# Optimization experiments

Hardware: AMD Instinct MI355X
Metric: run time of the kernel (lower is better)

The kernel has to match this reference:

```python
import jax, jax.numpy as jnp
import numpy as np

N, E, H, IN = 4096, 65536, 256, 16
N_BLOCKS, N_SUB = 3, 2
IE = 2 * H + 2  # edge-mlp input: h[row] ++ h[col] ++ edge_attr(2)
NORM_FACTOR = 100.0


def setup_inputs() -> dict:
    key = jax.random.key(0)
    ks = jax.random.split(key, 24)
    G = N_BLOCKS * N_SUB  # 6 GCLs total

    def p(k, shape, fan_in, gain=1.0):
        return gain * jax.random.normal(k, shape, jnp.float32) / np.sqrt(fan_in)

    return {
        "h": jax.random.normal(ks[0], (N, IN), jnp.float32),
        "x": jax.random.normal(ks[1], (N, 3), jnp.float32),
        "edge_index": jax.random.randint(ks[2], (2, E), 0, N),
        # embedding in/out
        "emb_w": p(ks[3], (IN, H), IN), "emb_b": jnp.zeros((H,), jnp.float32),
        "out_w": p(ks[4], (H, IN), H), "out_b": jnp.zeros((IN,), jnp.float32),
        # GCL edge MLP (stacked over the 6 GCLs)
        "edge_w1": p(ks[5], (G, IE, H), IE), "edge_b1": jnp.zeros((G, H), jnp.float32),
        "edge_w2": p(ks[6], (G, H, H), H), "edge_b2": jnp.zeros((G, H), jnp.float32),
        # GCL node MLP
        "node_w1": p(ks[7], (G, 2 * H, H), 2 * H), "node_b1": jnp.zeros((G, H), jnp.float32),
        "node_w2": p(ks[8], (G, H, H), H), "node_b2": jnp.zeros((G, H), jnp.float32),
        # EquivariantUpdate coord MLP (stacked over 3 blocks); last layer xavier gain=0.001, no bias
        "coord_w1": p(ks[9], (N_BLOCKS, IE, H), IE), "coord_b1": jnp.zeros((N_BLOCKS, H), jnp.float32),
        "coord_w2": p(ks[10], (N_BLOCKS, H, H), H), "coord_b2": jnp.zeros((N_BLOCKS, H), jnp.float32),
        "coord_w3": p(ks[11], (N_BLOCKS, H, 1), H, gain=0.001),
    }


def reference(h, x, edge_index, emb_w, emb_b, out_w, out_b,
              edge_w1, edge_b1, edge_w2, edge_b2,
              node_w1, node_b1, node_w2, node_b2,
              coord_w1, coord_b1, coord_w2, coord_b2, coord_w3):
    row, col = edge_index[0], edge_index[1]
    n_nodes = h.shape[0]

    def seg_sum(data):  # unsorted_segment_sum with 'sum' aggregation / normalization_factor
        return jax.ops.segment_sum(data, row, num_segments=n_nodes) / NORM_FACTOR

    def coord2diff(xc):  # norm_constant = 1
        d = xc[row] - xc[col]                      # [E,3]
        radial = jnp.sum(d * d, axis=1, keepdims=True)  # [E,1]
        cd = d / (jnp.sqrt(radial + 1e-8) + 1.0)
        return radial, cd

    dist0, _ = coord2diff(x)          # EGNN-level distances (from initial coords)
    h = h @ emb_w + emb_b             # node embedding

    gi = 0
    for b in range(N_BLOCKS):
        radial, coord_diff = coord2diff(x)
        ea = jnp.concatenate([radial, dist0], axis=1)   # [E,2] edge_attr
        for _ in range(N_SUB):  # GCL sublayers
            m = jnp.concatenate([h[row], h[col], ea], axis=1)           # [E, 2H+2]
            m = jax.nn.silu(m @ edge_w1[gi] + edge_b1[gi])
            m = jax.nn.silu(m @ edge_w2[gi] + edge_b2[gi])              # [E, H]
            agg = seg_sum(m)                                            # [N, H]
            u = jnp.concatenate([h, agg], axis=1)                       # [N, 2H]
            u = jax.nn.silu(u @ node_w1[gi] + node_b1[gi])
            h = h + u @ node_w2[gi] + node_b2[gi]                       # residual node update
            gi += 1
        # EquivariantUpdate (tanh=False)
        t = jnp.concatenate([h[row], h[col], ea], axis=1)
        t = jax.nn.silu(t @ coord_w1[b] + coord_b1[b])
        t = jax.nn.silu(t @ coord_w2[b] + coord_b2[b])
        trans = coord_diff * (t @ coord_w3[b])                          # [E,3]
        x = x + seg_sum(trans)

    h = h @ out_w + out_b
    return h, x
```

## Files before the change

### kernel.cpp

```cpp
#include <hip/hip_runtime.h>
#include <hip/hip_bf16.h>
#include <cstdint>
#include <cstddef>

#define NN 4096
#define NE 65536
#define HD 256

typedef __attribute__((ext_vector_type(4))) float f32x4;
typedef __attribute__((ext_vector_type(8))) __bf16 bf16x8;

static __device__ __forceinline__ float silu_f(float v) {
  float e = __builtin_amdgcn_exp2f(v * -1.442695040888963f);
  return v * __builtin_amdgcn_rcpf(1.f + e);
}

struct TJob { const float* src; __bf16* dst; int K; int N; };
struct TJobs { TJob j[39]; };

__global__ __launch_bounds__(256) void k_transpose(TJobs jobs) {
  TJob jb = jobs.j[blockIdx.z];
  int k0 = blockIdx.x << 5, n0 = blockIdx.y << 5;
  if (k0 >= jb.K || n0 >= jb.N) return;
  __shared__ float t[32][33];
  int tx = threadIdx.x & 31, ty = threadIdx.x >> 5;
#pragma unroll
  for (int r = ty; r < 32; r += 8)
    t[r][tx] = jb.src[(size_t)(k0 + r) * jb.N + n0 + tx];
  __syncthreads();
#pragma unroll
  for (int r = ty; r < 32; r += 8)
    jb.dst[(size_t)(n0 + r) * jb.K + k0 + tx] = (__bf16)t[tx][r];
}

__global__ __launch_bounds__(256) void k_hist(const int* __restrict__ ei, int* __restrict__ cnt) {
  int e = blockIdx.x * 256 + threadIdx.x;
  atomicAdd(&cnt[ei[e]], 1);
}

__global__ __launch_bounds__(1024) void k_scan(const int* __restrict__ cnt, int* __restrict__ offs,
                                               int* __restrict__ cursor) {
  __shared__ int tmp[1024];
  int tid = threadIdx.x;
  int v[4]; int s = 0;
#pragma unroll
  for (int i = 0; i < 4; i++) { v[i] = cnt[tid * 4 + i]; s += v[i]; }
  tmp[tid] = s;
  __syncthreads();
  for (int o = 1; o < 1024; o <<= 1) {
    int t = (tid >= o) ? tmp[tid - o] : 0;
    __syncthreads();
    tmp[tid] += t;
    __syncthreads();
  }
  int base = (tid > 0) ? tmp[tid - 1] : 0;
#pragma unroll
  for (int i = 0; i < 4; i++) {
    offs[tid * 4 + i] = base; cursor[tid * 4 + i] = base; base += v[i];
  }
  if (tid == 1023) offs[4096] = base;
}

__global__ __launch_bounds__(256) void k_scatter(const int* __restrict__ ei, int* __restrict__ cursor,
                                                 int* __restrict__ elist) {
  int e = blockIdx.x * 256 + threadIdx.x;
  int pos = atomicAdd(&cursor[ei[e]], 1);
  elist[pos] = e;
}

__global__ __launch_bounds__(256) void k_csrinit(const int* __restrict__ elist, const int* __restrict__ ei,
                                                 const float* __restrict__ x, int* __restrict__ rowp,
                                                 int* __restrict__ colp, float* __restrict__ d0p,
                                                 float* __restrict__ xc) {
  int i = blockIdx.x * 256 + threadIdx.x;
  if (i < NN * 3) xc[i] = x[i];
  int e = elist[i];
  int r = ei[e], c = ei[NE + e];
  rowp[i] = r; colp[i] = c;
  float dx = x[r * 3 + 0] - x[c * 3 + 0];
  float dy = x[r * 3 + 1] - x[c * 3 + 1];
  float dz = x[r * 3 + 2] - x[c * 3 + 2];
  d0p[i] = dx * dx + dy * dy + dz * dz;
}

__global__ __launch_bounds__(256) void k_geo(const int* __restrict__ rowp, const int* __restrict__ colp,
                                             const float* __restrict__ x, float* __restrict__ radp,
                                             float* __restrict__ cdp) {
  int i = blockIdx.x * 256 + threadIdx.x;
  int r = rowp[i], c = colp[i];
  float dx = x[r * 3 + 0] - x[c * 3 + 0];
  float dy = x[r * 3 + 1] - x[c * 3 + 1];
  float dz = x[r * 3 + 2] - x[c * 3 + 2];
  float rad = dx * dx + dy * dy + dz * dz;
  radp[i] = rad;
  float inv = 1.f / (sqrtf(rad + 1e-8f) + 1.f);
  cdp[i * 3 + 0] = dx * inv; cdp[i * 3 + 1] = dy * inv; cdp[i * 3 + 2] = dz * inv;
}

__global__ __launch_bounds__(256) void k_embed(const float* __restrict__ h0, const float* __restrict__ W,
                                               const float* __restrict__ b, float* __restrict__ hf,
                                               __bf16* __restrict__ h16) {
  int n = blockIdx.x, c = threadIdx.x;
  float s = b[c];
#pragma unroll
  for (int i = 0; i < 16; i++) s += h0[n * 16 + i] * W[i * 256 + c];
  hf[(size_t)n * HD + c] = s;
  h16[(size_t)n * HD + c] = (__bf16)s;
}

__global__ __launch_bounds__(256) void k_mkbias(const float* __restrict__ eb1, const float* __restrict__ cb1,
                                                float* __restrict__ bias512) {
  int i = blockIdx.x * 256 + threadIdx.x;
  int g = i >> 9, r = i & 511;
  float v = 0.f;
  if (r < 256) v = (g < 6) ? eb1[g * 256 + r] : cb1[(g - 6) * 256 + r];
  bias512[i] = v;
}

__global__ __launch_bounds__(256) void k_segsum(const __bf16* __restrict__ m2p, const int* __restrict__ offs,
                                                __bf16* __restrict__ agg16) {
  __shared__ float sd[8][256];
  int n = blockIdx.x, t = threadIdx.x;
  int g = t >> 5, l = t & 31;
  int c0 = l << 3;
  float a[8] = {};
  int ib = offs[n], ie = offs[n + 1];
  for (int i = ib + g; i < ie; i += 8) {
    bf16x8 v = *(const bf16x8*)(m2p + (size_t)i * 256 + c0);
#pragma unroll
    for (int j = 0; j < 8; j++) a[j] += (float)v[j];
  }
#pragma unroll
  for (int j = 0; j < 8; j++) sd[g][c0 + j] = a[j];
  __syncthreads();
  float s = 0.f;
#pragma unroll
  for (int j = 0; j < 8; j++) s += sd[j][t];
  agg16[(size_t)n * 256 + t] = (__bf16)(s * 0.01f);
}

__global__ __launch_bounds__(256) void k_xupd(const float* __restrict__ transp, const int* __restrict__ offs,
                                              float* __restrict__ xc) {
  int n = blockIdx.x * 256 + threadIdx.x;
  if (n >= NN) return;
  float a0 = 0.f, a1 = 0.f, a2 = 0.f;
  int i1 = offs[n + 1];
  for (int i = offs[n]; i < i1; i++) {
    a0 += transp[i * 3 + 0]; a1 += transp[i * 3 + 1]; a2 += transp[i * 3 + 2];
  }
  xc[n * 3 + 0] += a0 * 0.01f;
  xc[n * 3 + 1] += a1 * 0.01f;
  xc[n * 3 + 2] += a2 * 0.01f;
}

__global__ __launch_bounds__(256) void k_out(const float* __restrict__ hf, const float* __restrict__ W,
                                             const float* __restrict__ b, const float* __restrict__ xc,
                                             float* __restrict__ out) {
  int t = blockIdx.x * 256 + threadIdx.x;
  if (blockIdx.x < 256) {
    int n = t >> 4, j = t & 15;
    float s = b[j];
    for (int c = 0; c < 256; c++) s += hf[(size_t)n * HD + c] * W[c * 16 + j];
    out[n * 16 + j] = s;
  } else {
    int i = t - NN * 16;
    if (i < NN * 3) out[NN * 16 + i] = xc[i];
  }
}

template <int EPI>
__global__ __launch_bounds__(512, 4) void k_edgeblk(
    const __bf16* __restrict__ PQ, const int* __restrict__ rowp, const int* __restrict__ colp,
    const float* __restrict__ radp, const float* __restrict__ d0p,
    const float* __restrict__ w1r, const float* __restrict__ w1d,
    const __bf16* __restrict__ Bt, const float* __restrict__ b2,
    __bf16* __restrict__ m2p,
    const float* __restrict__ w3, const float* __restrict__ cdp, float* __restrict__ transp) {
  __shared__ alignas(16) char smem[37888];
  float*  wgt = (float*)smem;
  __bf16* Bs0 = (__bf16*)(smem + 4096);
  __bf16* Bs1 = (__bf16*)(smem + 4096 + 16384);
  float*  reds = (float*)(smem + 4096);

  const int tid = threadIdx.x;
  const int lane = tid & 63;
  const int w = tid >> 6;
  const int l15 = lane & 15;
  const int kg = lane >> 4;
  const int R0 = blockIdx.x * 128;
  const int rowg = R0 + w * 16 + l15;

  const __bf16* pBase = PQ + (size_t)rowp[rowg] * 512;
  const __bf16* qBase = PQ + (size_t)colp[rowg] * 512 + 256;
  const float rad = radp[rowg], dd0 = d0p[rowg];

  if (tid < 256) {
    wgt[tid]       = w1r[tid];
    wgt[256 + tid] = w1d[tid];
  } else {
    int t2 = tid - 256;
    wgt[512 + t2] = b2[t2];
    if (EPI == 1) wgt[768 + t2] = w3[t2];
  }

  int srcOff[2];
#pragma unroll
  for (int q = 0; q < 2; q++) {
    int s = q * 512 + tid;
    int n = s >> 2, g = s & 3;
    srcOff[q] = n * 256 + ((g ^ ((n >> 1) & 3)) << 3);
  }
  const int dstE0 = (0 * 512 + (w << 6)) * 8;
  const int dstE1 = (1 * 512 + (w << 6)) * 8;

  __builtin_amdgcn_global_load_lds((const unsigned int*)(Bt + srcOff[0]),
                                   (unsigned int*)(Bs0 + dstE0), 16, 0, 0);
  __builtin_amdgcn_global_load_lds((const unsigned int*)(Bt + srcOff[1]),
                                   (unsigned int*)(Bs0 + dstE1), 16, 0, 0);
  bf16x8 pvc = *(const bf16x8*)(pBase + kg * 8);
  bf16x8 qvc = *(const bf16x8*)(qBase + kg * 8);
  __syncthreads();

  f32x4 acc[16] = {};

#pragma unroll
  for (int t = 0; t < 8; t++) {
    const __bf16* Bcur = (t & 1) ? Bs1 : Bs0;
    __bf16*       Bnxt = (t & 1) ? Bs0 : Bs1;
    bf16x8 pvn, qvn;
    if (t < 7) {
      int kt = (t + 1) * 32;
      __builtin_amdgcn_global_load_lds((const unsigned int*)(Bt + kt + srcOff[0]),
                                       (unsigned int*)(Bnxt + dstE0), 16, 0, 0);
      __builtin_amdgcn_global_load_lds((const unsigned int*)(Bt + kt + srcOff[1]),
                                       (unsigned int*)(Bnxt + dstE1), 16, 0, 0);
      pvn = *(const bf16x8*)(pBase + kt + kg * 8);
      qvn = *(const bf16x8*)(qBase + kt + kg * 8);
    }
    const int k0 = t * 32 + kg * 8;
    f32x4 wr0 = *(const f32x4*)&wgt[k0],       wr1 = *(const f32x4*)&wgt[k0 + 4];
    f32x4 wd0 = *(const f32x4*)&wgt[256 + k0], wd1 = *(const f32x4*)&wgt[256 + k0 + 4];
    bf16x8 af;
#pragma unroll
    for (int j = 0; j < 4; j++)
      af[j] = (__bf16)silu_f((float)pvc[j] + (float)qvc[j] + rad * wr0[j] + dd0 * wd0[j]);
#pragma unroll
    for (int j = 0; j < 4; j++)
      af[4 + j] = (__bf16)silu_f((float)pvc[4 + j] + (float)qvc[4 + j] + rad * wr1[j] + dd0 * wd1[j]);
    __builtin_amdgcn_s_setprio(1);
#pragma unroll
    for (int fn = 0; fn < 16; fn++) {
      int n = fn * 16 + l15;
      bf16x8 bf = *(const bf16x8*)&Bcur[n * 32 + ((kg ^ ((n >> 1) & 3)) << 3)];
      acc[fn] = __builtin_amdgcn_mfma_f32_16x16x32_bf16(af, bf, acc[fn], 0, 0, 0);
    }
    __builtin_amdgcn_s_setprio(0);
    if (t < 7) { pvc = pvn; qvc = qvn; }
    __syncthreads();
  }

  if (EPI == 0) {
    __bf16* ep = (__bf16*)(smem + 4096 + w * 4224);
#pragma unroll
    for (int p = 0; p < 2; p++) {
      if ((kg >> 1) == p) {
        int rl = (kg & 1) * 4;
#pragma unroll
        for (int fn = 0; fn < 16; fn++) {
          int col = fn * 16 + l15;
          float bv = wgt[512 + col];
#pragma unroll
          for (int j = 0; j < 4; j++)
            ep[(rl + j) * 264 + col] = (__bf16)silu_f(acc[fn][j] + bv);
        }
      }
      __syncthreads();
#pragma unroll
      for (int i = 0; i < 4; i++) {
        int r = i * 2 + (lane >> 5);
        int g = lane & 31;
        uint4 v = *(const uint4*)&ep[r * 264 + g * 8];
        *(uint4*)(m2p + ((size_t)(R0 + w * 16 + p * 8 + r)) * 256 + g * 8) = v;
      }
      __syncthreads();
    }
  } else {
    float s[4] = {0.f, 0.f, 0.f, 0.f};
#pragma unroll
    for (int fn = 0; fn < 16; fn++) {
      int col = fn * 16 + l15;
      float bv = wgt[512 + col], wv = wgt[768 + col];
#pragma unroll
      for (int j = 0; j < 4; j++)
        s[j] += silu_f(acc[fn][j] + bv) * wv;
    }
#pragma unroll
    for (int off = 1; off < 16; off <<= 1)
#pragma unroll
      for (int j = 0; j < 4; j++)
        s[j] += __shfl_xor(s[j], off, 64);
    __syncthreads();
    if (l15 == 0) {
#pragma unroll
      for (int j = 0; j < 4; j++)
        reds[w * 16 + kg * 4 + j] = s[j];
    }
    __syncthreads();
    if (tid < 128) {
      float sv = reds[tid];
      size_t i = (size_t)R0 + tid;
      transp[i * 3 + 0] = cdp[i * 3 + 0] * sv;
      transp[i * 3 + 1] = cdp[i * 3 + 1] * sv;
      transp[i * 3 + 2] = cdp[i * 3 + 2] * sv;
    }
  }
}

template <int EPI, int SPLIT>
__global__ __launch_bounds__(256) void k_gemm64(const __bf16* __restrict__ A, const __bf16* __restrict__ A2,
                                                const __bf16* __restrict__ Bt,
                                                const float* __restrict__ bias, __bf16* __restrict__ outb,
                                                float* __restrict__ outf, int M, int N, int K) {
  constexpr int BM = 64, BN = 64, BK = 64;
  __shared__ __bf16 As[2][BM * BK];
  __shared__ __bf16 Bs[2][BN * BK];
  const int tid = threadIdx.x;
  const int lane = tid & 63;
  const int wave = tid >> 6;
  const int wm = wave >> 1, wn = wave & 1;
  const size_t m0 = (size_t)blockIdx.x * BM;
  const size_t n0 = (size_t)blockIdx.y * BN;
  const int r0 = tid >> 3, g0 = tid & 7;
  const int gs0 = (g0 ^ (r0 & 7)) << 3;
  const int Astride = SPLIT ? 256 : K;

  f32x4 acc[2][2] = {};
  const int NT = K >> 6;

  {
    uint4 a0 = *(const uint4*)(A + (m0 + r0) * Astride + g0 * 8);
    uint4 a1 = *(const uint4*)(A + (m0 + r0 + 32) * Astride + g0 * 8);
    uint4 b0 = *(const uint4*)(Bt + (n0 + r0) * K + g0 * 8);
    uint4 b1 = *(const uint4*)(Bt + (n0 + r0 + 32) * K + g0 * 8);
    *(uint4*)&As[0][r0 * BK + gs0] = a0;
    *(uint4*)&As[0][(r0 + 32) * BK + gs0] = a1;
    *(uint4*)&Bs[0][r0 * BK + gs0] = b0;
    *(uint4*)&Bs[0][(r0 + 32) * BK + gs0] = b1;
  }
  __syncthreads();

  int buf = 0;
  for (int t = 0; t < NT; ++t) {
    const bool has = (t + 1 < NT);
    uint4 a0, a1, b0, b1;
    if (has) {
      int kt = (t + 1) << 6;
      const __bf16* Ab;
      int ko;
      if (SPLIT) { Ab = (kt < 256) ? A : A2; ko = kt & 255; }
      else       { Ab = A; ko = kt; }
      a0 = *(const uint4*)(Ab + (m0 + r0) * Astride + ko + g0 * 8);
      a1 = *(const uint4*)(Ab + (m0 + r0 + 32) * Astride + ko + g0 * 8);
      b0 = *(const uint4*)(Bt + (n0 + r0) * K + kt + g0 * 8);
      b1 = *(const uint4*)(Bt + (n0 + r0 + 32) * K + kt + g0 * 8);
    }
#pragma unroll
    for (int ks = 0; ks < BK; ks += 32) {
      const int kg = (ks >> 3) + (lane >> 4);
      bf16x8 af[2], bfv[2];
#pragma unroll
      for (int fm = 0; fm < 2; fm++) {
        int r = wm * 32 + fm * 16 + (lane & 15);
        af[fm] = *(const bf16x8*)&As[buf][r * BK + ((kg ^ (r & 7)) << 3)];
      }
#pragma unroll
      for (int fn = 0; fn < 2; fn++) {
        int r = wn * 32 + fn * 16 + (lane & 15);
        bfv[fn] = *(const bf16x8*)&Bs[buf][r * BK + ((kg ^ (r & 7)) << 3)];
      }
#pragma unroll
      for (int fm = 0; fm < 2; fm++)
#pragma unroll
        for (int fn = 0; fn < 2; fn++)
          acc[fm][fn] = __builtin_amdgcn_mfma_f32_16x16x32_bf16(af[fm], bfv[fn], acc[fm][fn], 0, 0, 0);
    }
    if (has) {
      *(uint4*)&As[buf ^ 1][r0 * BK + gs0] = a0;
      *(uint4*)&As[buf ^ 1][(r0 + 32) * BK + gs0] = a1;
      *(uint4*)&Bs[buf ^ 1][r0 * BK + gs0] = b0;
      *(uint4*)&Bs[buf ^ 1][(r0 + 32) * BK + gs0] = b1;
    }
    __syncthreads();
    buf ^= 1;
  }

#pragma unroll
  for (int fm = 0; fm < 2; fm++) {
#pragma unroll
    for (int fn = 0; fn < 2; fn++) {
      const size_t col = n0 + wn * 32 + fn * 16 + (lane & 15);
      float bv = (EPI == 4) ? 0.f : bias[col];
#pragma unroll
      for (int j = 0; j < 4; j++) {
        size_t row = m0 + wm * 32 + fm * 16 + ((lane >> 4) << 2) + j;
        size_t idx = row * (size_t)N + col;
        float v = acc[fm][fn][j] + bv;
        if (EPI == 1) {
          outb[idx] = (__bf16)silu_f(v);
        } else if (EPI == 2) {
          float nh = outf[idx] + v;
          outf[idx] = nh;
          outb[idx] = (__bf16)nh;
        } else {
          outb[idx] = (__bf16)v;
        }
      }
    }
  }
}

extern "C" void kernel_launch(void* const* d_in, const int* in_sizes, int n_in,
                              void* d_out, int out_size, void* d_ws, size_t ws_size,
                              hipStream_t stream) {
  const float* h_in    = (const float*)d_in[0];
  const float* x_in    = (const float*)d_in[1];
  const int*   ei      = (const int*)d_in[2];
  const float* emb_w   = (const float*)d_in[3];
  const float* emb_b   = (const float*)d_in[4];
  const float* out_w   = (const float*)d_in[5];
  const float* out_b   = (const float*)d_in[6];
  const float* edge_w1 = (const float*)d_in[7];
  const float* edge_b1 = (const float*)d_in[8];
  const float* edge_w2 = (const float*)d_in[9];
  const float* edge_b2 = (const float*)d_in[10];
  const float* node_w1 = (const float*)d_in[11];
  const float* node_b1 = (const float*)d_in[12];
  const float* node_w2 = (const float*)d_in[13];
  const float* node_b2 = (const float*)d_in[14];
  const float* coord_w1 = (const float*)d_in[15];
  const float* coord_b1 = (const float*)d_in[16];
  const float* coord_w2 = (const float*)d_in[17];
  const float* coord_b2 = (const float*)d_in[18];
  const float* coord_w3 = (const float*)d_in[19];

  char* p = (char*)d_ws;
  auto alloc = [&](size_t bytes) -> void* {
    void* r = (void*)p;
    p += (bytes + 255) & ~(size_t)255;
    return r;
  };
  __bf16* e1T  = (__bf16*)alloc((size_t)6 * 512 * 256 * 2);
  __bf16* e2T  = (__bf16*)alloc((size_t)6 * 256 * 256 * 2);
  __bf16* n1T  = (__bf16*)alloc((size_t)6 * 256 * 512 * 2);
  __bf16* n2T  = (__bf16*)alloc((size_t)6 * 256 * 256 * 2);
  __bf16* c1T  = (__bf16*)alloc((size_t)3 * 512 * 256 * 2);
  __bf16* c2T  = (__bf16*)alloc((size_t)3 * 256 * 256 * 2);
  __bf16* h16  = (__bf16*)alloc((size_t)NN * HD * 2);
  __bf16* PQ16 = (__bf16*)alloc((size_t)NN * 512 * 2);
  __bf16* m2p  = (__bf16*)alloc((size_t)NE * HD * 2);
  __bf16* agg16 = (__bf16*)alloc((size_t)NN * HD * 2);
  __bf16* u    = (__bf16*)alloc((size_t)NN * HD * 2);
  float* hf    = (float*)alloc((size_t)NN * HD * 4);
  float* xc    = (float*)alloc((size_t)NN * 3 * 4);
  float* d0p   = (float*)alloc((size_t)NE * 4);
  float* radp  = (float*)alloc((size_t)NE * 4);
  float* cdp   = (float*)alloc((size_t)NE * 3 * 4);
  float* transp = (float*)alloc((size_t)NE * 3 * 4);
  float* bias512 = (float*)alloc((size_t)9 * 512 * 4);
  int* cnt     = (int*)alloc((size_t)NN * 4);
  int* offs    = (int*)alloc((size_t)(NN + 1) * 4);
  int* cursor  = (int*)alloc((size_t)NN * 4);
  int* elist   = (int*)alloc((size_t)NE * 4);
  int* rowp    = (int*)alloc((size_t)NE * 4);
  int* colp    = (int*)alloc((size_t)NE * 4);

  TJobs jobs;
  int nj = 0;
  for (int gi = 0; gi < 6; gi++) {
    jobs.j[nj++] = { edge_w1 + (size_t)gi * 514 * 256,             e1T + (size_t)gi * 512 * 256,             256, 256 };
    jobs.j[nj++] = { edge_w1 + (size_t)gi * 514 * 256 + 256 * 256, e1T + (size_t)gi * 512 * 256 + 256 * 256, 256, 256 };
    jobs.j[nj++] = { edge_w2 + (size_t)gi * 256 * 256,             e2T + (size_t)gi * 256 * 256,             256, 256 };
    jobs.j[nj++] = { node_w1 + (size_t)gi * 512 * 256,             n1T + (size_t)gi * 256 * 512,             512, 256 };
    jobs.j[nj++] = { node_w2 + (size_t)gi * 256 * 256,             n2T + (size_t)gi * 256 * 256,             256, 256 };
  }
  for (int b = 0; b < 3; b++) {
    jobs.j[nj++] = { coord_w1 + (size_t)b * 514 * 256,             c1T + (size_t)b * 512 * 256,              256, 256 };
    jobs.j[nj++] = { coord_w1 + (size_t)b * 514 * 256 + 256 * 256, c1T + (size_t)b * 512 * 256 + 256 * 256,  256, 256 };
    jobs.j[nj++] = { coord_w2 + (size_t)b * 256 * 256,             c2T + (size_t)b * 256 * 256,              256, 256 };
  }

  hipMemsetAsync(cnt, 0, (size_t)NN * 4, stream);
  k_transpose<<<dim3(16, 8, 39), 256, 0, stream>>>(jobs);
  k_hist<<<NE / 256, 256, 0, stream>>>(ei, cnt);
  k_scan<<<1, 1024, 0, stream>>>(cnt, offs, cursor);
  k_scatter<<<NE / 256, 256, 0, stream>>>(ei, cursor, elist);
  k_csrinit<<<NE / 256, 256, 0, stream>>>(elist, ei, x_in, rowp, colp, d0p, xc);
  k_mkbias<<<18, 256, 0, stream>>>(edge_b1, coord_b1, bias512);
  k_embed<<<NN, 256, 0, stream>>>(h_in, emb_w, emb_b, hf, h16);

  int gi = 0;
  for (int b = 0; b < 3; b++) {
    k_geo<<<NE / 256, 256, 0, stream>>>(rowp, colp, xc, radp, cdp);
    for (int s = 0; s < 2; s++, gi++) {
      const float* w1 = edge_w1 + (size_t)gi * 514 * 256;
      k_gemm64<5, 0><<<dim3(64, 8), 256, 0, stream>>>(
          h16, nullptr, e1T + (size_t)gi * 512 * 256, bias512 + gi * 512, PQ16, nullptr, NN, 512, 256);
      k_edgeblk<0><<<NE / 128, 512, 0, stream>>>(
          PQ16, rowp, colp, radp, d0p, w1 + 512 * 256, w1 + 513 * 256,
          e2T + (size_t)gi * 256 * 256, edge_b2 + gi * 256, m2p, nullptr, nullptr, nullptr);
      k_segsum<<<NN, 256, 0, stream>>>(m2p, offs, agg16);
      k_gemm64<1, 1><<<dim3(64, 4), 256, 0, stream>>>(
          h16, agg16, n1T + (size_t)gi * 256 * 512, node_b1 + gi * 256, u, nullptr, NN, 256, 512);
      k_gemm64<2, 0><<<dim3(64, 4), 256, 0, stream>>>(
          u, nullptr, n2T + (size_t)gi * 256 * 256, node_b2 + gi * 256, h16, hf, NN, 256, 256);
    }
    const float* w1c = coord_w1 + (size_t)b * 514 * 256;
    k_gemm64<5, 0><<<dim3(64, 8), 256, 0, stream>>>(
        h16, nullptr, c1T + (size_t)b * 512 * 256, bias512 + (6 + b) * 512, PQ16, nullptr, NN, 512, 256);
    k_edgeblk<1><<<NE / 128, 512, 0, stream>>>(
        PQ16, rowp, colp, radp, d0p, w1c + 512 * 256, w1c + 513 * 256,
        c2T + (size_t)b * 256 * 256, coord_b2 + b * 256, nullptr,
        coord_w3 + (size_t)b * 256, cdp, transp);
    k_xupd<<<NN / 256, 256, 0, stream>>>(transp, offs, xc);
  }
  k_out<<<256 + 48, 256, 0, stream>>>(hf, out_w, out_b, xc, (float*)d_out);
}
```

Baseline: 460.0 us.

## Fuse segment-sum into edge MLP epilogue via fp32 atomics on sorted rows

```diff
diff --git a/kernel.cpp b/kernel.cpp
--- a/kernel.cpp
+++ b/kernel.cpp
@@ -9,6 +9,8 @@
 
 typedef __attribute__((ext_vector_type(4))) float f32x4;
 typedef __attribute__((ext_vector_type(8))) __bf16 bf16x8;
+typedef __attribute__((ext_vector_type(4))) __bf16 bf16x4;
+union U8 { bf16x8 h; uint4 u; };
 
 static __device__ __forceinline__ float silu_f(float v) {
   float e = __builtin_amdgcn_exp2f(v * -1.442695040888963f);
@@ -71,6 +73,7 @@
 __global__ __launch_bounds__(256) void k_csrinit(const int* __restrict__ elist, const int* __restrict__ ei,
                                                  const float* __restrict__ x, int* __restrict__ rowp,
                                                  int* __restrict__ colp, float* __restrict__ d0p,
+                                                 float* __restrict__ radp, float* __restrict__ cdp,
                                                  float* __restrict__ xc) {
   int i = blockIdx.x * 256 + threadIdx.x;
   if (i < NN * 3) xc[i] = x[i];
@@ -80,7 +83,11 @@
   float dx = x[r * 3 + 0] - x[c * 3 + 0];
   float dy = x[r * 3 + 1] - x[c * 3 + 1];
   float dz = x[r * 3 + 2] - x[c * 3 + 2];
-  d0p[i] = dx * dx + dy * dy + dz * dz;
+  float rad = dx * dx + dy * dy + dz * dz;
+  d0p[i] = rad;
+  radp[i] = rad;
+  float inv = 1.f / (sqrtf(rad + 1e-8f) + 1.f);
+  cdp[i * 3 + 0] = dx * inv; cdp[i * 3 + 1] = dy * inv; cdp[i * 3 + 2] = dz * inv;
 }
 
 __global__ __launch_bounds__(256) void k_geo(const int* __restrict__ rowp, const int* __restrict__ colp,
@@ -117,28 +124,6 @@
   bias512[i] = v;
 }
 
-__global__ __launch_bounds__(256) void k_segsum(const __bf16* __restrict__ m2p, const int* __restrict__ offs,
-                                                __bf16* __restrict__ agg16) {
-  __shared__ float sd[8][256];
-  int n = blockIdx.x, t = threadIdx.x;
-  int g = t >> 5, l = t & 31;
-  int c0 = l << 3;
-  float a[8] = {};
-  int ib = offs[n], ie = offs[n + 1];
-  for (int i = ib + g; i < ie; i += 8) {
-    bf16x8 v = *(const bf16x8*)(m2p + (size_t)i * 256 + c0);
-#pragma unroll
-    for (int j = 0; j < 8; j++) a[j] += (float)v[j];
-  }
-#pragma unroll
-  for (int j = 0; j < 8; j++) sd[g][c0 + j] = a[j];
-  __syncthreads();
-  float s = 0.f;
-#pragma unroll
-  for (int j = 0; j < 8; j++) s += sd[j][t];
-  agg16[(size_t)n * 256 + t] = (__bf16)(s * 0.01f);
-}
-
 __global__ __launch_bounds__(256) void k_xupd(const float* __restrict__ transp, const int* __restrict__ offs,
                                               float* __restrict__ xc) {
   int n = blockIdx.x * 256 + threadIdx.x;
@@ -174,7 +159,7 @@
     const float* __restrict__ radp, const float* __restrict__ d0p,
     const float* __restrict__ w1r, const float* __restrict__ w1d,
     const __bf16* __restrict__ Bt, const float* __restrict__ b2,
-    __bf16* __restrict__ m2p,
+    float* __restrict__ aggf,
     const float* __restrict__ w3, const float* __restrict__ cdp, float* __restrict__ transp) {
   __shared__ alignas(16) char smem[37888];
   float*  wgt = (float*)smem;
@@ -261,6 +246,7 @@
 
   if (EPI == 0) {
     __bf16* ep = (__bf16*)(smem + 4096 + w * 4224);
+    const int c0 = lane * 4;
 #pragma unroll
     for (int p = 0; p < 2; p++) {
       if ((kg >> 1) == p) {
@@ -275,12 +261,28 @@
         }
       }
       __syncthreads();
-#pragma unroll
-      for (int i = 0; i < 4; i++) {
-        int r = i * 2 + (lane >> 5);
-        int g = lane & 31;
-        uint4 v = *(const uint4*)&ep[r * 264 + g * 8];
-        *(uint4*)(m2p + ((size_t)(R0 + w * 16 + p * 8 + r)) * 256 + g * 8) = v;
+      {
+        const int base = R0 + w * 16 + p * 8;
+        int cur = rowp[base];
+        bf16x4 v0 = *(const bf16x4*)&ep[c0];
+        float s0 = (float)v0[0], s1 = (float)v0[1], s2 = (float)v0[2], s3 = (float)v0[3];
+#pragma unroll
+        for (int r = 1; r < 8; r++) {
+          int nid = rowp[base + r];
+          bf16x4 v = *(const bf16x4*)&ep[r * 264 + c0];
+          if (nid != cur) {
+            float* d = aggf + (size_t)cur * 256 + c0;
+            unsafeAtomicAdd(d + 0, s0); unsafeAtomicAdd(d + 1, s1);
+            unsafeAtomicAdd(d + 2, s2); unsafeAtomicAdd(d + 3, s3);
+            cur = nid;
+            s0 = (float)v[0]; s1 = (float)v[1]; s2 = (float)v[2]; s3 = (float)v[3];
+          } else {
+            s0 += (float)v[0]; s1 += (float)v[1]; s2 += (float)v[2]; s3 += (float)v[3];
+          }
+        }
+        float* d = aggf + (size_t)cur * 256 + c0;
+        unsafeAtomicAdd(d + 0, s0); unsafeAtomicAdd(d + 1, s1);
+        unsafeAtomicAdd(d + 2, s2); unsafeAtomicAdd(d + 3, s3);
       }
       __syncthreads();
     }
@@ -316,11 +318,12 @@
   }
 }
 
-template <int EPI, int SPLIT>
+template <int EPI, int SPLIT, int A2F>
 __global__ __launch_bounds__(256) void k_gemm64(const __bf16* __restrict__ A, const __bf16* __restrict__ A2,
                                                 const __bf16* __restrict__ Bt,
                                                 const float* __restrict__ bias, __bf16* __restrict__ outb,
-                                                float* __restrict__ outf, int M, int N, int K) {
+                                                float* __restrict__ outf, int M, int N, int K,
+                                                float* __restrict__ aggz) {
   constexpr int BM = 64, BN = 64, BK = 64;
   __shared__ __bf16 As[2][BM * BK];
   __shared__ __bf16 Bs[2][BN * BK];
@@ -334,6 +337,13 @@
   const int gs0 = (g0 ^ (r0 & 7)) << 3;
   const int Astride = SPLIT ? 256 : K;
 
+  if (EPI == 5 && aggz) {
+    int bid = blockIdx.y * gridDim.x + blockIdx.x;
+    float4 z = {0.f, 0.f, 0.f, 0.f};
+    float* dst = aggz + (size_t)bid * 2048 + tid * 8;
+    *(float4*)dst = z; *(float4*)(dst + 4) = z;
+  }
+
   f32x4 acc[2][2] = {};
   const int NT = K >> 6;
 
@@ -355,12 +365,25 @@
     uint4 a0, a1, b0, b1;
     if (has) {
       int kt = (t + 1) << 6;
-      const __bf16* Ab;
-      int ko;
-      if (SPLIT) { Ab = (kt < 256) ? A : A2; ko = kt & 255; }
-      else       { Ab = A; ko = kt; }
-      a0 = *(const uint4*)(Ab + (m0 + r0) * Astride + ko + g0 * 8);
-      a1 = *(const uint4*)(Ab + (m0 + r0 + 32) * Astride + ko + g0 * 8);
+      int ko = SPLIT ? (kt & 255) : kt;
+      if (SPLIT && A2F && kt >= 256) {
+        const float* af2 = (const float*)A2;
+        f32x4 u0 = *(const f32x4*)(af2 + (m0 + r0) * 256 + ko + g0 * 8);
+        f32x4 u1 = *(const f32x4*)(af2 + (m0 + r0) * 256 + ko + g0 * 8 + 4);
+        f32x4 u2 = *(const f32x4*)(af2 + (m0 + r0 + 32) * 256 + ko + g0 * 8);
+        f32x4 u3 = *(const f32x4*)(af2 + (m0 + r0 + 32) * 256 + ko + g0 * 8 + 4);
+        U8 x0, x1;
+#pragma unroll
+        for (int j = 0; j < 4; j++) {
+          x0.h[j] = (__bf16)(u0[j] * 0.01f); x0.h[4 + j] = (__bf16)(u1[j] * 0.01f);
+          x1.h[j] = (__bf16)(u2[j] * 0.01f); x1.h[4 + j] = (__bf16)(u3[j] * 0.01f);
+        }
+        a0 = x0.u; a1 = x1.u;
+      } else {
+        const __bf16* Ab = (SPLIT && kt >= 256) ? A2 : A;
+        a0 = *(const uint4*)(Ab + (m0 + r0) * Astride + ko + g0 * 8);
+        a1 = *(const uint4*)(Ab + (m0 + r0 + 32) * Astride + ko + g0 * 8);
+      }
       b0 = *(const uint4*)(Bt + (n0 + r0) * K + kt + g0 * 8);
       b1 = *(const uint4*)(Bt + (n0 + r0 + 32) * K + kt + g0 * 8);
     }
@@ -399,7 +422,7 @@
 #pragma unroll
     for (int fn = 0; fn < 2; fn++) {
       const size_t col = n0 + wn * 32 + fn * 16 + (lane & 15);
-      float bv = (EPI == 4) ? 0.f : bias[col];
+      float bv = bias[col];
 #pragma unroll
       for (int j = 0; j < 4; j++) {
         size_t row = m0 + wm * 32 + fm * 16 + ((lane >> 4) << 2) + j;
@@ -457,9 +480,8 @@
   __bf16* c2T  = (__bf16*)alloc((size_t)3 * 256 * 256 * 2);
   __bf16* h16  = (__bf16*)alloc((size_t)NN * HD * 2);
   __bf16* PQ16 = (__bf16*)alloc((size_t)NN * 512 * 2);
-  __bf16* m2p  = (__bf16*)alloc((size_t)NE * HD * 2);
-  __bf16* agg16 = (__bf16*)alloc((size_t)NN * HD * 2);
   __bf16* u    = (__bf16*)alloc((size_t)NN * HD * 2);
+  float* aggf  = (float*)alloc((size_t)NN * HD * 4);
   float* hf    = (float*)alloc((size_t)NN * HD * 4);
   float* xc    = (float*)alloc((size_t)NN * 3 * 4);
   float* d0p   = (float*)alloc((size_t)NE * 4);
@@ -494,34 +516,37 @@
   k_hist<<<NE / 256, 256, 0, stream>>>(ei, cnt);
   k_scan<<<1, 1024, 0, stream>>>(cnt, offs, cursor);
   k_scatter<<<NE / 256, 256, 0, stream>>>(ei, cursor, elist);
-  k_csrinit<<<NE / 256, 256, 0, stream>>>(elist, ei, x_in, rowp, colp, d0p, xc);
+  k_csrinit<<<NE / 256, 256, 0, stream>>>(elist, ei, x_in, rowp, colp, d0p, radp, cdp, xc);
   k_mkbias<<<18, 256, 0, stream>>>(edge_b1, coord_b1, bias512);
   k_embed<<<NN, 256, 0, stream>>>(h_in, emb_w, emb_b, hf, h16);
 
   int gi = 0;
   for (int b = 0; b < 3; b++) {
-    k_geo<<<NE / 256, 256, 0, stream>>>(rowp, colp, xc, radp, cdp);
     for (int s = 0; s < 2; s++, gi++) {
       const float* w1 = edge_w1 + (size_t)gi * 514 * 256;
-      k_gemm64<5, 0><<<dim3(64, 8), 256, 0, stream>>>(
-          h16, nullptr, e1T + (size_t)gi * 512 * 256, bias512 + gi * 512, PQ16, nullptr, NN, 512, 256);
+      k_gemm64<5, 0, 0><<<dim3(64, 8), 256, 0, stream>>>(
+          h16, nullptr, e1T + (size_t)gi * 512 * 256, bias512 + gi * 512, PQ16, nullptr,
+          NN, 512, 256, aggf);
       k_edgeblk<0><<<NE / 128, 512, 0, stream>>>(
           PQ16, rowp, colp, radp, d0p, w1 + 512 * 256, w1 + 513 * 256,
-          e2T + (size_t)gi * 256 * 256, edge_b2 + gi * 256, m2p, nullptr, nullptr, nullptr);
-      k_segsum<<<NN, 256, 0, stream>>>(m2p, offs, agg16);
-      k_gemm64<1, 1><<<dim3(64, 4), 256, 0, stream>>>(
-          h16, agg16, n1T + (size_t)gi * 256 * 512, node_b1 + gi * 256, u, nullptr, NN, 256, 512);
-      k_gemm64<2, 0><<<dim3(64, 4), 256, 0, stream>>>(
-          u, nullptr, n2T + (size_t)gi * 256 * 256, node_b2 + gi * 256, h16, hf, NN, 256, 256);
+          e2T + (size_t)gi * 256 * 256, edge_b2 + gi * 256, aggf, nullptr, nullptr, nullptr);
+      k_gemm64<1, 1, 1><<<dim3(64, 4), 256, 0, stream>>>(
+          h16, (const __bf16*)aggf, n1T + (size_t)gi * 256 * 512, node_b1 + gi * 256, u, nullptr,
+          NN, 256, 512, nullptr);
+      k_gemm64<2, 0, 0><<<dim3(64, 4), 256, 0, stream>>>(
+          u, nullptr, n2T + (size_t)gi * 256 * 256, node_b2 + gi * 256, h16, hf,
+          NN, 256, 256, nullptr);
     }
     const float* w1c = coord_w1 + (size_t)b * 514 * 256;
-    k_gemm64<5, 0><<<dim3(64, 8), 256, 0, stream>>>(
-        h16, nullptr, c1T + (size_t)b * 512 * 256, bias512 + (6 + b) * 512, PQ16, nullptr, NN, 512, 256);
+    k_gemm64<5, 0, 0><<<dim3(64, 8), 256, 0, stream>>>(
+        h16, nullptr, c1T + (size_t)b * 512 * 256, bias512 + (6 + b) * 512, PQ16, nullptr,
+        NN, 512, 256, nullptr);
     k_edgeblk<1><<<NE / 128, 512, 0, stream>>>(
         PQ16, rowp, colp, radp, d0p, w1c + 512 * 256, w1c + 513 * 256,
         c2T + (size_t)b * 256 * 256, coord_b2 + b * 256, nullptr,
         coord_w3 + (size_t)b * 256, cdp, transp);
     k_xupd<<<NN / 256, 256, 0, stream>>>(transp, offs, xc);
+    if (b < 2) k_geo<<<NE / 256, 256, 0, stream>>>(rowp, colp, xc, radp, cdp);
   }
   k_out<<<256 + 48, 256, 0, stream>>>(hf, out_w, out_b, xc, (float*)d_out);
 }
```

Result: slower. 608.0 us (+32.2%).

## Fuse node MLP GEMMs into single kernel with shared-memory intermediate

Applied to the files above, without the earlier changes.

```diff
diff --git a/kernel.cpp b/kernel.cpp
--- a/kernel.cpp
+++ b/kernel.cpp
@@ -316,11 +316,71 @@
   }
 }
 
-template <int EPI, int SPLIT>
-__global__ __launch_bounds__(256) void k_gemm64(const __bf16* __restrict__ A, const __bf16* __restrict__ A2,
+__global__ __launch_bounds__(512) void k_nodemlp(
+    const __bf16* __restrict__ h16, const __bf16* __restrict__ agg16,
+    const __bf16* __restrict__ W1t, const float* __restrict__ b1,
+    const __bf16* __restrict__ W2t, const float* __restrict__ b2,
+    __bf16* __restrict__ h16o, float* __restrict__ hf) {
+  __shared__ __bf16 us[16 * 264];
+  const int tid = threadIdx.x;
+  const int lane = tid & 63;
+  const int w = tid >> 6;
+  const int l15 = lane & 15;
+  const int kg = lane >> 4;
+  const int R0 = blockIdx.x * 16;
+  const int colb = w * 32;
+
+  f32x4 acc[2] = {};
+#pragma unroll
+  for (int ks = 0; ks < 16; ks++) {
+    const __bf16* Asrc = (ks < 8)
+        ? (h16  + (size_t)(R0 + l15) * 256 + ks * 32 + kg * 8)
+        : (agg16 + (size_t)(R0 + l15) * 256 + (ks - 8) * 32 + kg * 8);
+    bf16x8 av = *(const bf16x8*)Asrc;
+#pragma unroll
+    for (int fn = 0; fn < 2; fn++) {
+      bf16x8 bv = *(const bf16x8*)(W1t + (size_t)(colb + fn * 16 + l15) * 512 + ks * 32 + kg * 8);
+      acc[fn] = __builtin_amdgcn_mfma_f32_16x16x32_bf16(av, bv, acc[fn], 0, 0, 0);
+    }
+  }
+#pragma unroll
+  for (int fn = 0; fn < 2; fn++) {
+    int col = colb + fn * 16 + l15;
+    float bv = b1[col];
+#pragma unroll
+    for (int j = 0; j < 4; j++)
+      us[(kg * 4 + j) * 264 + col] = (__bf16)silu_f(acc[fn][j] + bv);
+  }
+  __syncthreads();
+
+  f32x4 acc2[2] = {};
+#pragma unroll
+  for (int ks = 0; ks < 8; ks++) {
+    bf16x8 av = *(const bf16x8*)&us[l15 * 264 + ks * 32 + kg * 8];
+#pragma unroll
+    for (int fn = 0; fn < 2; fn++) {
+      bf16x8 bv = *(const bf16x8*)(W2t + (size_t)(colb + fn * 16 + l15) * 256 + ks * 32 + kg * 8);
+      acc2[fn] = __builtin_amdgcn_mfma_f32_16x16x32_bf16(av, bv, acc2[fn], 0, 0, 0);
+    }
+  }
+#pragma unroll
+  for (int fn = 0; fn < 2; fn++) {
+    int col = colb + fn * 16 + l15;
+    float bv = b2[col];
+#pragma unroll
+    for (int j = 0; j < 4; j++) {
+      size_t idx = (size_t)(R0 + kg * 4 + j) * 256 + col;
+      float nh = hf[idx] + acc2[fn][j] + bv;
+      hf[idx] = nh;
+      h16o[idx] = (__bf16)nh;
+    }
+  }
+}
+
+__global__ __launch_bounds__(256) void k_gemm64(const __bf16* __restrict__ A,
                                                 const __bf16* __restrict__ Bt,
-                                                const float* __restrict__ bias, __bf16* __restrict__ outb,
-                                                float* __restrict__ outf, int M, int N, int K) {
+                                                const float* __restrict__ bias,
+                                                __bf16* __restrict__ outb, int M, int N, int K) {
   constexpr int BM = 64, BN = 64, BK = 64;
   __shared__ __bf16 As[2][BM * BK];
   __shared__ __bf16 Bs[2][BN * BK];
@@ -332,14 +392,13 @@
   const size_t n0 = (size_t)blockIdx.y * BN;
   const int r0 = tid >> 3, g0 = tid & 7;
   const int gs0 = (g0 ^ (r0 & 7)) << 3;
-  const int Astride = SPLIT ? 256 : K;
 
   f32x4 acc[2][2] = {};
   const int NT = K >> 6;
 
   {
-    uint4 a0 = *(const uint4*)(A + (m0 + r0) * Astride + g0 * 8);
-    uint4 a1 = *(const uint4*)(A + (m0 + r0 + 32) * Astride + g0 * 8);
+    uint4 a0 = *(const uint4*)(A + (m0 + r0) * K + g0 * 8);
+    uint4 a1 = *(const uint4*)(A + (m0 + r0 + 32) * K + g0 * 8);
     uint4 b0 = *(const uint4*)(Bt + (n0 + r0) * K + g0 * 8);
     uint4 b1 = *(const uint4*)(Bt + (n0 + r0 + 32) * K + g0 * 8);
     *(uint4*)&As[0][r0 * BK + gs0] = a0;
@@ -355,12 +414,8 @@
     uint4 a0, a1, b0, b1;
     if (has) {
       int kt = (t + 1) << 6;
-      const __bf16* Ab;
-      int ko;
-      if (SPLIT) { Ab = (kt < 256) ? A : A2; ko = kt & 255; }
-      else       { Ab = A; ko = kt; }
-      a0 = *(const uint4*)(Ab + (m0 + r0) * Astride + ko + g0 * 8);
-      a1 = *(const uint4*)(Ab + (m0 + r0 + 32) * Astride + ko + g0 * 8);
+      a0 = *(const uint4*)(A + (m0 + r0) * K + kt + g0 * 8);
+      a1 = *(const uint4*)(A + (m0 + r0 + 32) * K + kt + g0 * 8);
       b0 = *(const uint4*)(Bt + (n0 + r0) * K + kt + g0 * 8);
       b1 = *(const uint4*)(Bt + (n0 + r0 + 32) * K + kt + g0 * 8);
     }
@@ -399,21 +454,11 @@
 #pragma unroll
     for (int fn = 0; fn < 2; fn++) {
       const size_t col = n0 + wn * 32 + fn * 16 + (lane & 15);
-      float bv = (EPI == 4) ? 0.f : bias[col];
+      float bv = bias[col];
 #pragma unroll
       for (int j = 0; j < 4; j++) {
         size_t row = m0 + wm * 32 + fm * 16 + ((lane >> 4) << 2) + j;
-        size_t idx = row * (size_t)N + col;
-        float v = acc[fm][fn][j] + bv;
-        if (EPI == 1) {
-          outb[idx] = (__bf16)silu_f(v);
-        } else if (EPI == 2) {
-          float nh = outf[idx] + v;
-          outf[idx] = nh;
-          outb[idx] = (__bf16)nh;
-        } else {
-          outb[idx] = (__bf16)v;
-        }
+        outb[row * (size_t)N + col] = (__bf16)(acc[fm][fn][j] + bv);
       }
     }
   }
@@ -459,7 +504,6 @@
   __bf16* PQ16 = (__bf16*)alloc((size_t)NN * 512 * 2);
   __bf16* m2p  = (__bf16*)alloc((size_t)NE * HD * 2);
   __bf16* agg16 = (__bf16*)alloc((size_t)NN * HD * 2);
-  __bf16* u    = (__bf16*)alloc((size_t)NN * HD * 2);
   float* hf    = (float*)alloc((size_t)NN * HD * 4);
   float* xc    = (float*)alloc((size_t)NN * 3 * 4);
   float* d0p   = (float*)alloc((size_t)NE * 4);
@@ -503,20 +547,19 @@
     k_geo<<<NE / 256, 256, 0, stream>>>(rowp, colp, xc, radp, cdp);
     for (int s = 0; s < 2; s++, gi++) {
       const float* w1 = edge_w1 + (size_t)gi * 514 * 256;
-      k_gemm64<5, 0><<<dim3(64, 8), 256, 0, stream>>>(
-          h16, nullptr, e1T + (size_t)gi * 512 * 256, bias512 + gi * 512, PQ16, nullptr, NN, 512, 256);
+      k_gemm64<<<dim3(64, 8), 256, 0, stream>>>(
+          h16, e1T + (size_t)gi * 512 * 256, bias512 + gi * 512, PQ16, NN, 512, 256);
       k_edgeblk<0><<<NE / 128, 512, 0, stream>>>(
           PQ16, rowp, colp, radp, d0p, w1 + 512 * 256, w1 + 513 * 256,
           e2T + (size_t)gi * 256 * 256, edge_b2 + gi * 256, m2p, nullptr, nullptr, nullptr);
       k_segsum<<<NN, 256, 0, stream>>>(m2p, offs, agg16);
-      k_gemm64<1, 1><<<dim3(64, 4), 256, 0, stream>>>(
-          h16, agg16, n1T + (size_t)gi * 256 * 512, node_b1 + gi * 256, u, nullptr, NN, 256, 512);
-      k_gemm64<2, 0><<<dim3(64, 4), 256, 0, stream>>>(
-          u, nullptr, n2T + (size_t)gi * 256 * 256, node_b2 + gi * 256, h16, hf, NN, 256, 256);
+      k_nodemlp<<<NN / 16, 512, 0, stream>>>(
+          h16, agg16, n1T + (size_t)gi * 256 * 512, node_b1 + gi * 256,
+          n2T + (size_t)gi * 256 * 256, node_b2 + gi * 256, h16, hf);
     }
     const float* w1c = coord_w1 + (size_t)b * 514 * 256;
-    k_gemm64<5, 0><<<dim3(64, 8), 256, 0, stream>>>(
-        h16, nullptr, c1T + (size_t)b * 512 * 256, bias512 + (6 + b) * 512, PQ16, nullptr, NN, 512, 256);
+    k_gemm64<<<dim3(64, 8), 256, 0, stream>>>(
+        h16, c1T + (size_t)b * 512 * 256, bias512 + (6 + b) * 512, PQ16, NN, 512, 256);
     k_edgeblk<1><<<NE / 128, 512, 0, stream>>>(
         PQ16, rowp, colp, radp, d0p, w1c + 512 * 256, w1c + 513 * 256,
         c2T + (size_t)b * 256 * 256, coord_b2 + b * 256, nullptr,
```

Measured after the change: 479.0 us. 1.04x slower.
